# Kernel optimization log

Hardware: AMD Instinct MI355X
Metric: run time of the kernel (lower is better)

Reference implementation:

```python
import jax, jax.numpy as jnp
import numpy as np

DIM_IN = 1024
DIM_OUT = 1024
BATCH = 4
SEQ = 2048


def setup_inputs() -> dict:
    key = jax.random.key(0)
    kx, kq, kk, kv = jax.random.split(key, 4)
    scale = 1.0 / np.sqrt(DIM_IN)
    x = jax.random.normal(kx, (BATCH, SEQ, DIM_IN), dtype=jnp.float32)
    # Weights stored as [dim_in, dim_out] (transpose of torch Linear's [out, in]);
    # y = x @ W is equivalent math to torch's x @ W_t.T
    Wq = jax.random.normal(kq, (DIM_IN, DIM_OUT), dtype=jnp.float32) * scale
    Wk = jax.random.normal(kk, (DIM_IN, DIM_OUT), dtype=jnp.float32) * scale
    Wv = jax.random.normal(kv, (DIM_IN, DIM_OUT), dtype=jnp.float32) * scale
    return {"x": x, "Wq": Wq, "Wk": Wk, "Wv": Wv}


def reference(x, Wq, Wk, Wv):
    # x: [b, s, d_in]; single-head causal self-attention (dropout=0 -> identity)
    q = jnp.einsum("bsd,de->bse", x, Wq)
    k = jnp.einsum("bsd,de->bse", x, Wk)
    v = jnp.einsum("bsd,de->bse", x, Wv)
    dim_k = k.shape[-1]
    scores = jnp.einsum("bqe,bke->bqk", q, k) / jnp.sqrt(jnp.float32(dim_k))
    s = x.shape[1]
    causal = jnp.tril(jnp.ones((s, s), dtype=bool))  # True = keep
    scores = jnp.where(causal[None, :, :], scores, -jnp.inf)
    weights = jax.nn.softmax(scores, axis=-1)
    context = jnp.einsum("bqk,bke->bqe", weights, v)
    return context
```

## Files before the change

### kernel.cpp

```cpp
#include <hip/hip_runtime.h>
#include <cstdint>
#include <cstddef>
#include <type_traits>

typedef unsigned short u16;
typedef __bf16 bf16x8 __attribute__((ext_vector_type(8)));
typedef float f32x4 __attribute__((ext_vector_type(4)));

__device__ inline u16 f2b(float f) {
    uint32_t u = __builtin_bit_cast(uint32_t, f);
    u += 0x7FFFu + ((u >> 16) & 1u);
    return (u16)(u >> 16);
}

__device__ inline void gl2lds16(const u16* g, u16* l) {
    __builtin_amdgcn_global_load_lds(
        (const __attribute__((address_space(1))) void*)g,
        (__attribute__((address_space(3))) void*)l, 16, 0, 0);
}

template<int N> __device__ __forceinline__ void waitvm() {
    asm volatile("s_waitcnt vmcnt(%0)" :: "n"(N) : "memory");
}
__device__ __forceinline__ void waitlgkm0() {
    asm volatile("s_waitcnt lgkmcnt(0)" ::: "memory");
}
__device__ __forceinline__ void bar() {
    asm volatile("" ::: "memory");
    __builtin_amdgcn_s_barrier();
    asm volatile("" ::: "memory");
}

__global__ void convert_x_kernel(const float* __restrict__ x, u16* __restrict__ xb) {
    size_t i = ((size_t)blockIdx.x * 256 + threadIdx.x) * 4;
    float4 v = *(const float4*)(x + i);
    uint2 pack;
    pack.x = (uint32_t)f2b(v.x) | ((uint32_t)f2b(v.y) << 16);
    pack.y = (uint32_t)f2b(v.z) | ((uint32_t)f2b(v.w) << 16);
    *(uint2*)(xb + i) = pack;
}

__global__ void transpose_w_kernel(const float* __restrict__ Wq,
                                   const float* __restrict__ Wk,
                                   const float* __restrict__ Wv,
                                   u16* __restrict__ QKWT, u16* __restrict__ WvT) {
    __shared__ u16 t[32][33];
    const int z = blockIdx.z;
    const float* W = (z == 0) ? Wq : ((z == 1) ? Wk : Wv);
    u16* dst = (z == 0) ? QKWT : ((z == 1) ? QKWT + 1024 * 1024 : WvT);
    const float scale = (z == 0) ? 0.03125f : 1.0f;
    const int bx = blockIdx.x * 32;
    const int by = blockIdx.y * 32;
    const int tx = threadIdx.x, ty = threadIdx.y;
    #pragma unroll
    for (int r = 0; r < 32; r += 8)
        t[ty + r][tx] = f2b(W[(size_t)(by + ty + r) * 1024 + bx + tx] * scale);
    __syncthreads();
    #pragma unroll
    for (int r = 0; r < 32; r += 8)
        dst[(size_t)(bx + ty + r) * 1024 + (by + tx)] = t[tx][ty + r];
}

template<int NB, int EPI>
__device__ __forceinline__ void gemm8p(
    char* __restrict__ sm,
    const u16* __restrict__ A, int lda,
    const u16* __restrict__ B, int ldb,
    char* __restrict__ Cb, int ldc,
    int m0, int n0, int Kloc, float* __restrict__ lrow)
{
    constexpr int BREG  = NB / 2;
    constexpr int BUFSZ = (2 + BREG) * 16384;
    constexpr int BOFF  = 2 * 16384;
    constexpr int WVM   = NB;

    const int tid  = threadIdx.x;
    const int lane = tid & 63, wave = tid >> 6;
    const int wm = wave >> 2, wn = wave & 3;
    const int fl = lane & 15, fh = lane >> 4;

    const int sx = ((fl & 4) << 3) ^ ((fl & 1) << 6);

    const int rr0 = tid >> 3;
    const int kc  = ((tid & 7) * 8) ^ ((rr0 & 4) << 2) ^ ((rr0 & 1) << 5);
    const u16* sA0a = A + (size_t)(m0 + rr0) * lda + kc;
    const u16* sA0b = A + (size_t)(m0 + rr0 + 64) * lda + kc;
    const u16* sA1a = sA0a + (size_t)128 * lda;
    const u16* sA1b = sA0b + (size_t)128 * lda;
    const u16* sB0a = B + (size_t)(n0 + rr0) * ldb + kc;
    const u16* sB0b = B + (size_t)(n0 + rr0 + 64) * ldb + kc;
    const u16* sB1a = sB0a + (size_t)128 * ldb;
    const u16* sB1b = sB0b + (size_t)128 * ldb;

    auto st = [&](const u16* s0, const u16* s1, int reg, int t) {
        u16* d = (u16*)(void*)(sm + (size_t)(t & 1) * BUFSZ + reg * 16384)
                 + wave * 512;
        gl2lds16(s0 + (size_t)t * 64, d);
        gl2lds16(s1 + (size_t)t * 64, d + 4096);
    };

    const f32x4 vzero = {0.f, 0.f, 0.f, 0.f};
    f32x4 acc[8][NB];
    #pragma unroll
    for (int i = 0; i < 8; ++i)
        #pragma unroll
        for (int j = 0; j < NB; ++j) acc[i][j] = vzero;

    const int NT = Kloc >> 6;
    const int NPAIR = NT >> 1;

    st(sB0a, sB0b, 2, 0);
    if constexpr (NB == 4) st(sB1a, sB1b, 3, 0);
    st(sA0a, sA0b, 0, 0);
    st(sA1a, sA1b, 1, 0);
    st(sB0a, sB0b, 2, 1);
    if constexpr (NB == 4) st(sB1a, sB1b, 3, 1);
    waitvm<WVM>();
    bar();

    bf16x8 bfrag[NB][2];
    for (int pr = 0; pr < NPAIR; ++pr) {
        const int t0 = pr * 2;
        const bool last = (pr == NPAIR - 1);

        auto phase = [&](auto phc) {
            constexpr int PH = decltype(phc)::value;
            constexpr int q = PH & 3;
            constexpr int b = PH >> 2;
            if constexpr (q == 0) {
                #pragma unroll
                for (int nt = 0; nt < NB; ++nt)
                    #pragma unroll
                    for (int kk = 0; kk < 2; ++kk)
                        bfrag[nt][kk] = *(const bf16x8*)(sm + b * BUFSZ + BOFF
                            + wn * (NB * 2048) + nt * 2048 + fl * 128
                            + ((fh * 16 + kk * 64) ^ sx));
            }
            bf16x8 af[2][2];
            #pragma unroll
            for (int i = 0; i < 2; ++i)
                #pragma unroll
                for (int kk = 0; kk < 2; ++kk)
                    af[i][kk] = *(const bf16x8*)(sm + b * BUFSZ + wm * 16384
                        + (q * 2 + i) * 2048 + fl * 128
                        + ((fh * 16 + kk * 64) ^ sx));
            if constexpr (PH == 3) { if (last) waitvm<0>(); else waitvm<WVM>(); }
            if constexpr (PH == 7) { if (!last) waitvm<WVM>(); }
            waitlgkm0();
            bar();
            if constexpr (PH == 0) { st(sA0a, sA0b, 0, t0 + 1);
                                     st(sA1a, sA1b, 1, t0 + 1); }
            if constexpr (PH == 1) { if (!last) st(sB0a, sB0b, 2, t0 + 2); }
            if constexpr (PH == 2 && NB == 4) { if (!last) st(sB1a, sB1b, 3, t0 + 2); }
            if constexpr (PH == 4) { if (!last) st(sA0a, sA0b, 0, t0 + 2); }
            if constexpr (PH == 5) { if (!last) st(sA1a, sA1b, 1, t0 + 2); }
            if constexpr (PH == 6) { if (!last) st(sB0a, sB0b, 2, t0 + 3); }
            if constexpr (PH == 7 && NB == 4) { if (!last) st(sB1a, sB1b, 3, t0 + 3); }
            __builtin_amdgcn_s_setprio(1);
            #pragma unroll
            for (int i = 0; i < 2; ++i)
                #pragma unroll
                for (int nt = 0; nt < NB; ++nt)
                    #pragma unroll
                    for (int kk = 0; kk < 2; ++kk)
                        acc[q * 2 + i][nt] = __builtin_amdgcn_mfma_f32_16x16x32_bf16(
                            af[i][kk], bfrag[nt][kk], acc[q * 2 + i][nt], 0, 0, 0);
            __builtin_amdgcn_s_setprio(0);
        };
        phase(std::integral_constant<int, 0>{});
        phase(std::integral_constant<int, 1>{});
        phase(std::integral_constant<int, 2>{});
        phase(std::integral_constant<int, 3>{});
        phase(std::integral_constant<int, 4>{});
        phase(std::integral_constant<int, 5>{});
        phase(std::integral_constant<int, 6>{});
        phase(std::integral_constant<int, 7>{});
    }

    const int rbase = m0 + wm * 128 + fh * 4;
    const int cbase = n0 + wn * (NB * 16) + fl;
    if constexpr (EPI == 0) {
        u16* Cp = (u16*)Cb;
        #pragma unroll
        for (int mt = 0; mt < 8; ++mt)
            #pragma unroll
            for (int nt = 0; nt < NB; ++nt)
                #pragma unroll
                for (int r = 0; r < 4; ++r)
                    Cp[(size_t)(rbase + mt * 16 + r) * ldc + cbase + nt * 16] =
                        f2b(acc[mt][nt][r]);
    } else if constexpr (EPI == 2) {
        u16* Cp = (u16*)Cb;
        #pragma unroll
        for (int mt = 0; mt < 8; ++mt)
            #pragma unroll
            for (int r = 0; r < 4; ++r) {
                const int row = rbase + mt * 16 + r;
                float part = 0.f;
                #pragma unroll
                for (int nt = 0; nt < NB; ++nt) {
                    const int col = cbase + nt * 16;
                    float p = (col <= row) ? __expf(acc[mt][nt][r]) : 0.f;
                    part += p;
                    Cp[(size_t)row * ldc + col] = f2b(p);
                }
                #pragma unroll
                for (int off = 1; off < 16; off <<= 1)
                    part += __shfl_xor(part, off, 64);
                if (fl == 0) atomicAdd(lrow + row, part);
            }
    } else if constexpr (EPI == 3) {
        float* Cp = (float*)Cb;
        #pragma unroll
        for (int mt = 0; mt < 8; ++mt)
            #pragma unroll
            for (int r = 0; r < 4; ++r) {
                const int row = rbase + mt * 16 + r;
                const float inv = 1.0f / lrow[row];
                #pragma unroll
                for (int nt = 0; nt < NB; ++nt)
                    Cp[(size_t)row * ldc + cbase + nt * 16] = acc[mt][nt][r] * inv;
            }
    } else {
        float* Cp = (float*)Cb;
        #pragma unroll
        for (int mt = 0; mt < 8; ++mt)
            #pragma unroll
            for (int r = 0; r < 4; ++r) {
                const int row = rbase + mt * 16 + r;
                const float inv = 1.0f / lrow[row];
                #pragma unroll
                for (int nt = 0; nt < NB; ++nt)
                    atomicAdd(&Cp[(size_t)row * ldc + cbase + nt * 16],
                              acc[mt][nt][r] * inv);
            }
    }
}

__global__ __launch_bounds__(512, 2)
void proj_kernel(const u16* __restrict__ xb, const u16* __restrict__ QKWT,
                 const u16* __restrict__ WvT, u16* __restrict__ QK,
                 u16* __restrict__ Vt) {
    __shared__ __align__(16) char smem[131072];
    const int x = (int)blockIdx.x;
    if (x < 256) {
        const int bid = (x & 7) * 32 + (x >> 3);
        const int it = bid >> 3, jt = bid & 7;
        gemm8p<4, 0>(smem, xb, 1024, QKWT, 1024, (char*)QK, 2048,
                     it * 256, jt * 256, 1024, nullptr);
    } else {
        const int y = x - 256;
        const int bid = (y & 7) * 32 + (y >> 3);
        const int it = bid >> 6, jt = bid & 63;
        gemm8p<2, 0>(smem, WvT, 1024, xb, 1024, (char*)Vt, 8192,
                     it * 256, jt * 128, 1024, nullptr);
    }
}

__global__ __launch_bounds__(512, 2)
void scores_kernel(const u16* __restrict__ QK, u16* __restrict__ P,
                   float* __restrict__ l) {
    __shared__ __align__(16) char smem[131072];
    const int t = blockIdx.x, z = blockIdx.y;
    int it = (int)((sqrtf(8.0f * t + 1.0f) - 1.0f) * 0.5f);
    while ((it + 1) * (it + 2) / 2 <= t) ++it;
    while (it * (it + 1) / 2 > t) --it;
    const int jt = t - it * (it + 1) / 2;
    const u16* Qz = QK + (size_t)z * 2048 * 2048;
    const u16* Kz = Qz + 1024;
    u16* Pz = P + (size_t)z * 2048 * 2048;
    gemm8p<4, 2>(smem, Qz, 2048, Kz, 2048, (char*)Pz, 2048,
                 it * 256, jt * 256, 1024, l + (size_t)z * 2048);
}

__global__ __launch_bounds__(512, 2)
void out_kernel(const u16* __restrict__ P, const u16* __restrict__ Vt,
                float* __restrict__ out, float* __restrict__ l) {
    __shared__ __align__(16) char smem[98304];
    const int o = (int)blockIdx.x;
    int it, half, split, r;
    if (o < 256) { const int pc = o >> 5; r = o & 31; it = 7 - (pc >> 1);
                   half = pc & 1; split = 1; }
    else         { const int pc = (o - 256) >> 5; r = o & 31; it = 3 - pc;
                   half = 0; split = 0; }
    const int jt = r & 7, z = r >> 3;
    const int Kloc = split ? (it + 1) * 128 : (it + 1) * 256;
    const int k0 = half * Kloc;
    const u16* Pz = P + (size_t)z * 2048 * 2048 + k0;
    const u16* Vz = Vt + (size_t)z * 2048 + k0;
    char* C = (char*)(out + (size_t)z * 2048 * 1024);
    float* lz = l + (size_t)z * 2048;
    if (split)
        gemm8p<2, 4>(smem, Pz, 2048, Vz, 8192, C, 1024,
                     it * 256, jt * 128, Kloc, lz);
    else
        gemm8p<2, 3>(smem, Pz, 2048, Vz, 8192, C, 1024,
                     it * 256, jt * 128, Kloc, lz);
}

extern "C" void kernel_launch(void* const* d_in, const int* in_sizes, int n_in,
                              void* d_out, int out_size, void* d_ws, size_t ws_size,
                              hipStream_t stream) {
    (void)in_sizes; (void)n_in; (void)out_size; (void)ws_size;
    const float* x  = (const float*)d_in[0];
    const float* Wq = (const float*)d_in[1];
    const float* Wk = (const float*)d_in[2];
    const float* Wv = (const float*)d_in[3];
    float* out = (float*)d_out;

    const size_t MB = 1u << 20;
    char* ws = (char*)d_ws;
    u16* xb   = (u16*)(ws);
    u16* QKWT = (u16*)(ws + 16 * MB);
    u16* WvT  = (u16*)(ws + 20 * MB);
    u16* QK   = (u16*)(ws + 22 * MB);
    u16* Vt   = (u16*)(ws + 54 * MB);
    u16* P    = (u16*)(ws + 70 * MB);
    float* l  = (float*)(ws + 102 * MB);

    hipMemsetAsync(l, 0, 8192 * sizeof(float), stream);
    hipMemsetAsync(out, 0, (size_t)4 * 2048 * 1024 * sizeof(float), stream);
    convert_x_kernel<<<8192, 256, 0, stream>>>(x, xb);
    transpose_w_kernel<<<dim3(32, 32, 3), dim3(32, 8), 0, stream>>>(Wq, Wk, Wv, QKWT, WvT);

    proj_kernel<<<512, 512, 0, stream>>>(xb, QKWT, WvT, QK, Vt);
    scores_kernel<<<dim3(36, 4), 512, 0, stream>>>(QK, P, l);
    out_kernel<<<384, 512, 0, stream>>>(P, Vt, out, l);
}
```

Before: 254.5 us.

## Split Q/K into separate buffers and add alternate barrier schedule for scores GEMM

The projection kernel now writes Q and K into two contiguous 1024-wide buffers instead of one interleaved 2048-wide buffer, so the scores GEMM reads with stride 1024. The GEMM mainloop gains a SYNC template mode, used only by the scores kernel. In that mode the global->LDS loads are issued before the barrier and the explicit LDS-wait is dropped. A second barrier after the MFMAs replaces it. This aims to overlap load issue with synchronization, at the cost of an extra barrier per phase and a risk of LDS read/write hazards without lgkmcnt waits.

```diff
diff --git a/kernel.cpp b/kernel.cpp
--- a/kernel.cpp
+++ b/kernel.cpp
@@ -61,13 +61,13 @@
         dst[(size_t)(bx + ty + r) * 1024 + (by + tx)] = t[tx][ty + r];
 }
 
-template<int NB, int EPI>
+template<int NB, int EPI, int SYNC>
 __device__ __forceinline__ void gemm8p(
     char* __restrict__ sm,
     const u16* __restrict__ A, int lda,
     const u16* __restrict__ B, int ldb,
     char* __restrict__ Cb, int ldc,
-    int m0, int n0, int Kloc, float* __restrict__ lrow)
+    int m0, int n0, int n0c, int Kloc, float* __restrict__ lrow)
 {
     constexpr int BREG  = NB / 2;
     constexpr int BUFSZ = (2 + BREG) * 16384;
@@ -144,28 +144,47 @@
                     af[i][kk] = *(const bf16x8*)(sm + b * BUFSZ + wm * 16384
                         + (q * 2 + i) * 2048 + fl * 128
                         + ((fh * 16 + kk * 64) ^ sx));
-            if constexpr (PH == 3) { if (last) waitvm<0>(); else waitvm<WVM>(); }
-            if constexpr (PH == 7) { if (!last) waitvm<WVM>(); }
-            waitlgkm0();
-            bar();
-            if constexpr (PH == 0) { st(sA0a, sA0b, 0, t0 + 1);
-                                     st(sA1a, sA1b, 1, t0 + 1); }
-            if constexpr (PH == 1) { if (!last) st(sB0a, sB0b, 2, t0 + 2); }
-            if constexpr (PH == 2 && NB == 4) { if (!last) st(sB1a, sB1b, 3, t0 + 2); }
-            if constexpr (PH == 4) { if (!last) st(sA0a, sA0b, 0, t0 + 2); }
-            if constexpr (PH == 5) { if (!last) st(sA1a, sA1b, 1, t0 + 2); }
-            if constexpr (PH == 6) { if (!last) st(sB0a, sB0b, 2, t0 + 3); }
-            if constexpr (PH == 7 && NB == 4) { if (!last) st(sB1a, sB1b, 3, t0 + 3); }
-            __builtin_amdgcn_s_setprio(1);
-            #pragma unroll
-            for (int i = 0; i < 2; ++i)
-                #pragma unroll
-                for (int nt = 0; nt < NB; ++nt)
+
+            auto stages = [&]() {
+                if constexpr (PH == 0) { st(sA0a, sA0b, 0, t0 + 1);
+                                         st(sA1a, sA1b, 1, t0 + 1); }
+                if constexpr (PH == 1) { if (!last) st(sB0a, sB0b, 2, t0 + 2); }
+                if constexpr (PH == 2 && NB == 4) { if (!last) st(sB1a, sB1b, 3, t0 + 2); }
+                if constexpr (PH == 4) { if (!last) st(sA0a, sA0b, 0, t0 + 2); }
+                if constexpr (PH == 5) { if (!last) st(sA1a, sA1b, 1, t0 + 2); }
+                if constexpr (PH == 6) { if (!last) st(sB0a, sB0b, 2, t0 + 3); }
+                if constexpr (PH == 7 && NB == 4) { if (!last) st(sB1a, sB1b, 3, t0 + 3); }
+            };
+            auto vmwaits = [&]() {
+                if constexpr (PH == 3) { if (last) waitvm<0>(); else waitvm<WVM>(); }
+                if constexpr (PH == 7) { if (!last) waitvm<WVM>(); }
+            };
+            auto mfmas = [&]() {
+                __builtin_amdgcn_s_setprio(1);
+                #pragma unroll
+                for (int i = 0; i < 2; ++i)
                     #pragma unroll
-                    for (int kk = 0; kk < 2; ++kk)
-                        acc[q * 2 + i][nt] = __builtin_amdgcn_mfma_f32_16x16x32_bf16(
-                            af[i][kk], bfrag[nt][kk], acc[q * 2 + i][nt], 0, 0, 0);
-            __builtin_amdgcn_s_setprio(0);
+                    for (int nt = 0; nt < NB; ++nt)
+                        #pragma unroll
+                        for (int kk = 0; kk < 2; ++kk)
+                            acc[q * 2 + i][nt] = __builtin_amdgcn_mfma_f32_16x16x32_bf16(
+                                af[i][kk], bfrag[nt][kk], acc[q * 2 + i][nt], 0, 0, 0);
+                __builtin_amdgcn_s_setprio(0);
+            };
+
+            if constexpr (SYNC == 0) {
+                vmwaits();
+                waitlgkm0();
+                bar();
+                stages();
+                mfmas();
+            } else {
+                stages();
+                vmwaits();
+                bar();
+                mfmas();
+                bar();
+            }
         };
         phase(std::integral_constant<int, 0>{});
         phase(std::integral_constant<int, 1>{});
@@ -178,7 +197,7 @@
     }
 
     const int rbase = m0 + wm * 128 + fh * 4;
-    const int cbase = n0 + wn * (NB * 16) + fl;
+    const int cbase = n0c + wn * (NB * 16) + fl;
     if constexpr (EPI == 0) {
         u16* Cp = (u16*)Cb;
         #pragma unroll
@@ -239,38 +258,41 @@
 
 __global__ __launch_bounds__(512, 2)
 void proj_kernel(const u16* __restrict__ xb, const u16* __restrict__ QKWT,
-                 const u16* __restrict__ WvT, u16* __restrict__ QK,
-                 u16* __restrict__ Vt) {
+                 const u16* __restrict__ WvT, u16* __restrict__ Qb,
+                 u16* __restrict__ Kb, u16* __restrict__ Vt) {
     __shared__ __align__(16) char smem[131072];
     const int x = (int)blockIdx.x;
     if (x < 256) {
         const int bid = (x & 7) * 32 + (x >> 3);
         const int it = bid >> 3, jt = bid & 7;
-        gemm8p<4, 0>(smem, xb, 1024, QKWT, 1024, (char*)QK, 2048,
-                     it * 256, jt * 256, 1024, nullptr);
+        const int n0 = jt * 256;
+        char* C = (jt < 4) ? (char*)Qb : (char*)Kb;
+        const int n0c = (jt < 4) ? n0 : n0 - 1024;
+        gemm8p<4, 0, 0>(smem, xb, 1024, QKWT, 1024, C, 1024,
+                        it * 256, n0, n0c, 1024, nullptr);
     } else {
         const int y = x - 256;
         const int bid = (y & 7) * 32 + (y >> 3);
         const int it = bid >> 6, jt = bid & 63;
-        gemm8p<2, 0>(smem, WvT, 1024, xb, 1024, (char*)Vt, 8192,
-                     it * 256, jt * 128, 1024, nullptr);
+        gemm8p<2, 0, 0>(smem, WvT, 1024, xb, 1024, (char*)Vt, 8192,
+                        it * 256, jt * 128, jt * 128, 1024, nullptr);
     }
 }
 
 __global__ __launch_bounds__(512, 2)
-void scores_kernel(const u16* __restrict__ QK, u16* __restrict__ P,
-                   float* __restrict__ l) {
+void scores_kernel(const u16* __restrict__ Qb, const u16* __restrict__ Kb,
+                   u16* __restrict__ P, float* __restrict__ l) {
     __shared__ __align__(16) char smem[131072];
     const int t = blockIdx.x, z = blockIdx.y;
     int it = (int)((sqrtf(8.0f * t + 1.0f) - 1.0f) * 0.5f);
     while ((it + 1) * (it + 2) / 2 <= t) ++it;
     while (it * (it + 1) / 2 > t) --it;
     const int jt = t - it * (it + 1) / 2;
-    const u16* Qz = QK + (size_t)z * 2048 * 2048;
-    const u16* Kz = Qz + 1024;
+    const u16* Qz = Qb + (size_t)z * 2048 * 1024;
+    const u16* Kz = Kb + (size_t)z * 2048 * 1024;
     u16* Pz = P + (size_t)z * 2048 * 2048;
-    gemm8p<4, 2>(smem, Qz, 2048, Kz, 2048, (char*)Pz, 2048,
-                 it * 256, jt * 256, 1024, l + (size_t)z * 2048);
+    gemm8p<4, 2, 1>(smem, Qz, 1024, Kz, 1024, (char*)Pz, 2048,
+                    it * 256, jt * 256, jt * 256, 1024, l + (size_t)z * 2048);
 }
 
 __global__ __launch_bounds__(512, 2)
@@ -291,11 +313,11 @@
     char* C = (char*)(out + (size_t)z * 2048 * 1024);
     float* lz = l + (size_t)z * 2048;
     if (split)
-        gemm8p<2, 4>(smem, Pz, 2048, Vz, 8192, C, 1024,
-                     it * 256, jt * 128, Kloc, lz);
+        gemm8p<2, 4, 0>(smem, Pz, 2048, Vz, 8192, C, 1024,
+                        it * 256, jt * 128, jt * 128, Kloc, lz);
     else
-        gemm8p<2, 3>(smem, Pz, 2048, Vz, 8192, C, 1024,
-                     it * 256, jt * 128, Kloc, lz);
+        gemm8p<2, 3, 0>(smem, Pz, 2048, Vz, 8192, C, 1024,
+                        it * 256, jt * 128, jt * 128, Kloc, lz);
 }
 
 extern "C" void kernel_launch(void* const* d_in, const int* in_sizes, int n_in,
@@ -313,7 +335,8 @@
     u16* xb   = (u16*)(ws);
     u16* QKWT = (u16*)(ws + 16 * MB);
     u16* WvT  = (u16*)(ws + 20 * MB);
-    u16* QK   = (u16*)(ws + 22 * MB);
+    u16* Qb   = (u16*)(ws + 22 * MB);
+    u16* Kb   = (u16*)(ws + 38 * MB);
     u16* Vt   = (u16*)(ws + 54 * MB);
     u16* P    = (u16*)(ws + 70 * MB);
     float* l  = (float*)(ws + 102 * MB);
@@ -323,7 +346,7 @@
     convert_x_kernel<<<8192, 256, 0, stream>>>(x, xb);
     transpose_w_kernel<<<dim3(32, 32, 3), dim3(32, 8), 0, stream>>>(Wq, Wk, Wv, QKWT, WvT);
 
-    proj_kernel<<<512, 512, 0, stream>>>(xb, QKWT, WvT, QK, Vt);
-    scores_kernel<<<dim3(36, 4), 512, 0, stream>>>(QK, P, l);
+    proj_kernel<<<512, 512, 0, stream>>>(xb, QKWT, WvT, Qb, Kb, Vt);
+    scores_kernel<<<dim3(36, 4), 512, 0, stream>>>(Qb, Kb, P, l);
     out_kernel<<<384, 512, 0, stream>>>(P, Vt, out, l);
 }
```

Measured after the change: 253.6 us. About the same (-0.4%).
